# Kernel tuning notes

Measured on AMD Instinct MI355X. Metric: run time of the kernel, lower is better.

Reference implementation:

```python
import jax, jax.numpy as jnp
import numpy as np

B, LQ, LK, E, H = 8, 1024, 1024, 512, 8
D = E // H
NEG = -2.0**32 + 1  # padding value used by original torch code


def setup_inputs() -> dict:
    key = jax.random.key(0)
    ks = jax.random.split(key, 6)
    s = 0.02
    return {
        "x1": jax.random.normal(ks[0], (B, LQ, E), jnp.float32),
        "x2": jax.random.normal(ks[1], (B, LK, E), jnp.float32),
        "Wq": jax.random.normal(ks[2], (E, E), jnp.float32) * s,
        "bq": jnp.zeros((E,), jnp.float32),
        "Wk": jax.random.normal(ks[3], (E, E), jnp.float32) * s,
        "bk": jnp.zeros((E,), jnp.float32),
        "Wv": jax.random.normal(ks[4], (E, E), jnp.float32) * s,
        "bv": jnp.zeros((E,), jnp.float32),
    }


def _split_heads(t):
    # torch: cat(split(t, E//H, dim=2), dim=0) -> head-major [H, B, L, D]
    b, l, _ = t.shape
    return jnp.moveaxis(t.reshape(b, l, H, D), 2, 0)


def reference(x1, x2, Wq, bq, Wk, bk, Wv, bv):
    # ReLU-activated projections (nn.Linear: x @ W.T + b)
    q = jax.nn.relu(x1 @ Wq.T + bq)  # [B,LQ,E]
    k = jax.nn.relu(x2 @ Wk.T + bk)  # [B,LK,E]
    v = jax.nn.relu(x2 @ Wv.T + bv)  # [B,LK,E]

    q_, k_, v_ = _split_heads(q), _split_heads(k), _split_heads(v)  # [H,B,L,D]

    # scaled scores; original scales by sqrt(emb_size), not sqrt(d_head)
    scores = jnp.einsum('hbqd,hbkd->hbqk', q_, k_) / jnp.sqrt(jnp.float32(E))

    # sin-based key mask from raw x2
    key_mask = jnp.sin(jnp.abs(jnp.sum(x2, -1)))  # [B,LK]
    scores = jnp.where(key_mask[None, :, None, :] <= 0, NEG, scores)

    attn = jax.nn.softmax(scores, axis=-1)

    # sin-based query mask from raw x1, applied after softmax
    query_mask = jnp.sin(jnp.abs(jnp.sum(x1, -1)))  # [B,LQ]
    attn = attn * query_mask[None, :, :, None]

    out = jnp.einsum('hbqk,hbkd->hbqd', attn, v_)  # [H,B,LQ,D]
    out = jnp.moveaxis(out, 0, 2).reshape(B, LQ, E)  # merge heads back
    return out + q  # residual add with activated query projection
```

## Files before the change

### kernel.cpp

```cpp
#include <hip/hip_runtime.h>
#include <hip/hip_bf16.h>
#include <math.h>

typedef short bf16x8 __attribute__((ext_vector_type(8)));
typedef float f32x4 __attribute__((ext_vector_type(4)));
typedef unsigned int u32;
typedef unsigned short u16;

constexpr int Bb = 8, LQn = 1024, LKn = 1024, En = 512, Hn = 8, Dn = 64;
constexpr int Mtok = Bb * LQn;
constexpr float KCOEF = 0.06376246332977306f;

__device__ __forceinline__ u16 f2bf(float f) {
  u32 u = __builtin_bit_cast(u32, f);
  u32 r = (u + 0x7fffu + ((u >> 16) & 1u)) >> 16;
  return (u16)r;
}
__device__ __forceinline__ float bf2f(u16 h) {
  u32 u = ((u32)h) << 16;
  return __builtin_bit_cast(float, u);
}
__device__ __forceinline__ u16 f2bf_hw(float f) {
  return __builtin_bit_cast(u16, __float2bfloat16(f));
}

__device__ __forceinline__ void async_lds16(const void* gsrc, void* ldst) {
  __builtin_amdgcn_global_load_lds(
      (const __attribute__((address_space(1))) u32*)gsrc,
      (__attribute__((address_space(3))) u32*)ldst, 16, 0, 0);
}

__global__ void prep_kernel(const float* __restrict__ x1, const float* __restrict__ x2,
                            u16* __restrict__ x1b, u16* __restrict__ x2b,
                            float* __restrict__ qmask, float* __restrict__ kbias,
                            const float* __restrict__ Wq, const float* __restrict__ Wk,
                            const float* __restrict__ Wv, u16* __restrict__ wqb,
                            u16* __restrict__ wkb, u16* __restrict__ wvb) {
  int blk = blockIdx.x;
  if (blk < 4096) {
    int id = blk * 4 + (threadIdx.x >> 6);
    int lane = threadIdx.x & 63;
    const float* x; u16* xb; int row; bool isq;
    if (id < Mtok) { x = x1; xb = x1b; row = id; isq = true; }
    else           { x = x2; xb = x2b; row = id - Mtok; isq = false; }
    const float4* p = reinterpret_cast<const float4*>(x + (size_t)row * En);
    ushort4* ob = reinterpret_cast<ushort4*>(xb + (size_t)row * En);
    double s = 0.0;
#pragma unroll
    for (int j = 0; j < En / 256; ++j) {
      float4 v = p[lane + j * 64];
      s += (double)v.x + (double)v.y + (double)v.z + (double)v.w;
      ushort4 o;
      o.x = f2bf(v.x); o.y = f2bf(v.y); o.z = f2bf(v.z); o.w = f2bf(v.w);
      ob[lane + j * 64] = o;
    }
#pragma unroll
    for (int off = 32; off > 0; off >>= 1) s += __shfl_down(s, off, 64);
    if (lane == 0) {
      float sv = (float)sin(fabs(s));
      if (isq) qmask[row] = sv;
      else     kbias[row] = sv > 0.f ? 0.f : -3.0e38f;
    }
  } else {
    int n4 = En * En / 4;
    int j = (blk - 4096) * 256 + threadIdx.x;
    const float* src; u16* dst;
    if (j < n4) { src = Wq; dst = wqb; }
    else if (j < 2 * n4) { src = Wk; dst = wkb; j -= n4; }
    else { src = Wv; dst = wvb; j -= 2 * n4; }
    float4 v = reinterpret_cast<const float4*>(src)[j];
    ushort4 o;
    o.x = f2bf(v.x); o.y = f2bf(v.y); o.z = f2bf(v.z); o.w = f2bf(v.w);
    reinterpret_cast<ushort4*>(dst)[j] = o;
  }
}

template <int BIAS_ROW>
__device__ __forceinline__ void gemm_core(
    const u16* __restrict__ A, const u16* __restrict__ Bm,
    const float* __restrict__ bias, u16* __restrict__ C,
    int ldc, float coef, int row0, int col0) {
  constexpr int K = 512, BK = 64;
  __shared__ u16 sA[128 * BK];
  __shared__ u16 sB[128 * BK];
  int tid = threadIdx.x;
  int lane = tid & 63;
  int w = tid >> 6;
  int wm = w >> 2, wn = w & 3;
  int rgrp = lane >> 4, cidx = lane & 15;

  f32x4 acc[4][2];
#pragma unroll
  for (int mi = 0; mi < 4; ++mi)
#pragma unroll
    for (int ni = 0; ni < 2; ++ni) acc[mi][ni] = f32x4{0.f, 0.f, 0.f, 0.f};

  for (int kt = 0; kt < K / BK; ++kt) {
    int k0 = kt * BK;
    __syncthreads();
#pragma unroll
    for (int rr = 0; rr < 2; ++rr) {
      int cid = rr * 512 + tid;
      int r = cid >> 3, c = cid & 7;
      int cg = c ^ (r & 7);
      async_lds16(A + (size_t)(row0 + r) * K + k0 + cg * 8, &sA[cid * 8]);
    }
#pragma unroll
    for (int rr = 0; rr < 2; ++rr) {
      int cid = rr * 512 + tid;
      int r = cid >> 3, c = cid & 7;
      int cg = c ^ (r & 7);
      async_lds16(Bm + (size_t)(col0 + r) * K + k0 + cg * 8, &sB[cid * 8]);
    }
    __syncthreads();
#pragma unroll
    for (int kk = 0; kk < 2; ++kk) {
      bf16x8 a[4], b[2];
#pragma unroll
      for (int mi = 0; mi < 4; ++mi) {
        int row = wm * 64 + mi * 16 + cidx;
        a[mi] = *reinterpret_cast<const bf16x8*>(
            &sA[row * BK + ((kk * 4 + rgrp) ^ (row & 7)) * 8]);
      }
#pragma unroll
      for (int ni = 0; ni < 2; ++ni) {
        int row = wn * 32 + ni * 16 + cidx;
        b[ni] = *reinterpret_cast<const bf16x8*>(
            &sB[row * BK + ((kk * 4 + rgrp) ^ (row & 7)) * 8]);
      }
#pragma unroll
      for (int mi = 0; mi < 4; ++mi)
#pragma unroll
        for (int ni = 0; ni < 2; ++ni)
          acc[mi][ni] = __builtin_amdgcn_mfma_f32_16x16x32_bf16(a[mi], b[ni], acc[mi][ni], 0, 0, 0);
    }
  }
#pragma unroll
  for (int mi = 0; mi < 4; ++mi)
#pragma unroll
    for (int ni = 0; ni < 2; ++ni)
#pragma unroll
      for (int r = 0; r < 4; ++r) {
        int grow = row0 + wm * 64 + mi * 16 + rgrp * 4 + r;
        int gcol = col0 + wn * 32 + ni * 16 + cidx;
        float v = acc[mi][ni][r] + (BIAS_ROW ? bias[grow] : bias[gcol]);
        v = v > 0.f ? v : 0.f;
        C[(size_t)grow * ldc + gcol] = f2bf_hw(v * coef);
      }
}

__global__ __launch_bounds__(512, 6) void gemm3(
    const u16* __restrict__ x1b, const u16* __restrict__ wqb, const float* __restrict__ bq,
    u16* __restrict__ qbq,
    const u16* __restrict__ x2b, const u16* __restrict__ wkb, const float* __restrict__ bk,
    u16* __restrict__ kbk,
    const u16* __restrict__ wvb, const float* __restrict__ bv, u16* __restrict__ vtb) {
  int z = blockIdx.z;
  if (z == 0) {
    gemm_core<0>(x1b, wqb, bq, qbq, En, 1.0f, blockIdx.x * 128, blockIdx.y * 128);
  } else if (z == 1) {
    gemm_core<0>(x2b, wkb, bk, kbk, En, KCOEF, blockIdx.x * 128, blockIdx.y * 128);
  } else {
    gemm_core<1>(wvb, x2b, bv, vtb, Mtok, 1.0f, blockIdx.y * 128, blockIdx.x * 128);
  }
}

__global__ __launch_bounds__(256, 4) void attn_kernel(
    const u16* __restrict__ qb, const u16* __restrict__ kb, const u16* __restrict__ vtb,
    const float* __restrict__ kbias, const float* __restrict__ qmask,
    float* __restrict__ out) {
  __shared__ u16 sK[2][64 * 64];
  __shared__ u16 sV[2][64 * 64];
  __shared__ u16 sQP[64 * 64];
  int tid = threadIdx.x, lane = tid & 63, w = tid >> 6;
  int bh = blockIdx.x, qblk = blockIdx.y;
  int b = bh >> 3, h = bh & 7;
  int rgrp = lane >> 4, cidx = lane & 15;

  const u16* qbase = qb + ((size_t)(b * LQn) + qblk * 64) * En + h * Dn;
  const u16* kbase = kb + (size_t)(b * LKn) * En + h * Dn;
  const u16* vbase = vtb + (size_t)(h * Dn) * Mtok + b * LKn;
  const float* kmb = kbias + b * LKn;

  auto stageKV = [&](int kt, int buf) {
#pragma unroll
    for (int rr = 0; rr < 2; ++rr) {
      int cid = rr * 256 + tid;
      int r = cid >> 3, c = cid & 7;
      int cg = c ^ (r & 7);
      async_lds16(kbase + (size_t)(kt * 64 + r) * En + cg * 8, &sK[buf][cid * 8]);
      async_lds16(vbase + (size_t)r * Mtok + kt * 64 + cg * 8, &sV[buf][cid * 8]);
    }
  };

#pragma unroll
  for (int rr = 0; rr < 2; ++rr) {
    int cid = rr * 256 + tid;
    int r = cid >> 3, c = cid & 7;
    int cg = c ^ (r & 7);
    async_lds16(qbase + (size_t)r * En + cg * 8, &sQP[cid * 8]);
  }
  stageKV(0, 0);
  __syncthreads();

  bf16x8 qa0, qa1;
  {
    int row = w * 16 + cidx;
    qa0 = *reinterpret_cast<const bf16x8*>(&sQP[row * 64 + (rgrp ^ (row & 7)) * 8]);
    qa1 = *reinterpret_cast<const bf16x8*>(&sQP[row * 64 + ((4 + rgrp) ^ (row & 7)) * 8]);
  }

  f32x4 acc_o[4];
#pragma unroll
  for (int dt = 0; dt < 4; ++dt) acc_o[dt] = f32x4{0.f, 0.f, 0.f, 0.f};
  float den = 0.f;

  int prow = w * 16 + cidx;
  char* sPbyte = reinterpret_cast<char*>(sQP);

  for (int kt = 0; kt < LKn / 64; ++kt) {
    int cur = kt & 1;
    if (kt < LKn / 64 - 1) stageKV(kt + 1, cur ^ 1);
#pragma unroll
    for (int ktile = 0; ktile < 4; ++ktile) {
      int krow = ktile * 16 + cidx;
      bf16x8 kf0 = *reinterpret_cast<const bf16x8*>(
          &sK[cur][krow * 64 + (rgrp ^ (krow & 7)) * 8]);
      bf16x8 kf1 = *reinterpret_cast<const bf16x8*>(
          &sK[cur][krow * 64 + ((4 + rgrp) ^ (krow & 7)) * 8]);
      float4 km4 = *reinterpret_cast<const float4*>(&kmb[kt * 64 + ktile * 16 + rgrp * 4]);
      f32x4 s;
      s[0] = km4.x; s[1] = km4.y; s[2] = km4.z; s[3] = km4.w;
      s = __builtin_amdgcn_mfma_f32_16x16x32_bf16(kf0, qa0, s, 0, 0, 0);
      s = __builtin_amdgcn_mfma_f32_16x16x32_bf16(kf1, qa1, s, 0, 0, 0);
      float p0 = __builtin_amdgcn_exp2f(s[0]);
      float p1 = __builtin_amdgcn_exp2f(s[1]);
      float p2 = __builtin_amdgcn_exp2f(s[2]);
      float p3 = __builtin_amdgcn_exp2f(s[3]);
      den += (p0 + p1) + (p2 + p3);
      ushort4 pk;
      pk.x = f2bf_hw(p0); pk.y = f2bf_hw(p1); pk.z = f2bf_hw(p2); pk.w = f2bf_hw(p3);
      int gran = ktile * 2 + (rgrp >> 1);
      int boff = prow * 128 + ((gran ^ (prow & 7)) << 4) + ((rgrp & 1) << 3);
      *reinterpret_cast<ushort4*>(sPbyte + boff) = pk;
    }
    __builtin_amdgcn_s_setprio(1);
#pragma unroll
    for (int kk = 0; kk < 2; ++kk) {
      bf16x8 pa = *reinterpret_cast<const bf16x8*>(
          &sQP[prow * 64 + ((kk * 4 + rgrp) ^ (prow & 7)) * 8]);
#pragma unroll
      for (int dt = 0; dt < 4; ++dt) {
        int vrow = dt * 16 + cidx;
        bf16x8 vf = *reinterpret_cast<const bf16x8*>(
            &sV[cur][vrow * 64 + ((kk * 4 + rgrp) ^ (vrow & 7)) * 8]);
        acc_o[dt] = __builtin_amdgcn_mfma_f32_16x16x32_bf16(pa, vf, acc_o[dt], 0, 0, 0);
      }
    }
    __builtin_amdgcn_s_setprio(0);
    __syncthreads();
  }
  den += __shfl_xor(den, 16, 64);
  den += __shfl_xor(den, 32, 64);

  const float* qmb = qmask + (size_t)b * LQn + qblk * 64 + w * 16;
  const u16* qres = qbase + (size_t)(w * 16) * En;
  float* obase = out + ((size_t)(b * LQn) + qblk * 64 + w * 16) * En + h * Dn;
#pragma unroll
  for (int r = 0; r < 4; ++r) {
    int qr = rgrp * 4 + r;
    float denq = __shfl(den, qr, 64);
    float fac = qmb[qr] / denq;
#pragma unroll
    for (int dt = 0; dt < 4; ++dt) {
      float v = acc_o[dt][r] * fac + bf2f(qres[(size_t)qr * En + dt * 16 + cidx]);
      obase[(size_t)qr * En + dt * 16 + cidx] = v;
    }
  }
}

extern "C" void kernel_launch(void* const* d_in, const int* in_sizes, int n_in,
                              void* d_out, int out_size, void* d_ws, size_t ws_size,
                              hipStream_t stream) {
  const float* x1 = (const float*)d_in[0];
  const float* x2 = (const float*)d_in[1];
  const float* Wq = (const float*)d_in[2];
  const float* bq = (const float*)d_in[3];
  const float* Wk = (const float*)d_in[4];
  const float* bk = (const float*)d_in[5];
  const float* Wv = (const float*)d_in[6];
  const float* bv = (const float*)d_in[7];
  float* out = (float*)d_out;

  char* ws = (char*)d_ws;
  size_t o = 0;
  u16* x1b = (u16*)(ws + o); o += (size_t)Mtok * En * 2;
  u16* x2b = (u16*)(ws + o); o += (size_t)Mtok * En * 2;
  u16* wqb = (u16*)(ws + o); o += (size_t)En * En * 2;
  u16* wkb = (u16*)(ws + o); o += (size_t)En * En * 2;
  u16* wvb = (u16*)(ws + o); o += (size_t)En * En * 2;
  u16* qbq = (u16*)(ws + o); o += (size_t)Mtok * En * 2;
  u16* kbk = (u16*)(ws + o); o += (size_t)Mtok * En * 2;
  u16* vtb = (u16*)(ws + o); o += (size_t)Mtok * En * 2;
  float* kbias = (float*)(ws + o); o += (size_t)Mtok * 4;
  float* qmask = (float*)(ws + o); o += (size_t)Mtok * 4;

  prep_kernel<<<4864, 256, 0, stream>>>(x1, x2, x1b, x2b, qmask, kbias,
                                        Wq, Wk, Wv, wqb, wkb, wvb);

  dim3 g3(Mtok / 128, En / 128, 3);
  gemm3<<<g3, 512, 0, stream>>>(x1b, wqb, bq, qbq, x2b, wkb, bk, kbk, wvb, bv, vtb);

  dim3 ga(Bb * Hn, LQn / 64);
  attn_kernel<<<ga, 256, 0, stream>>>(qbq, kbk, vtb, kbias, qmask, out);
}
```

Before: 64.96 us.

## Process 128 query rows per attention block to reuse K/V tiles

```diff
diff --git a/kernel.cpp b/kernel.cpp
--- a/kernel.cpp
+++ b/kernel.cpp
@@ -165,19 +165,19 @@
   }
 }
 
-__global__ __launch_bounds__(256, 4) void attn_kernel(
+__global__ __launch_bounds__(256, 3) void attn_kernel(
     const u16* __restrict__ qb, const u16* __restrict__ kb, const u16* __restrict__ vtb,
     const float* __restrict__ kbias, const float* __restrict__ qmask,
     float* __restrict__ out) {
   __shared__ u16 sK[2][64 * 64];
   __shared__ u16 sV[2][64 * 64];
-  __shared__ u16 sQP[64 * 64];
+  __shared__ u16 sQP[128 * 64];
   int tid = threadIdx.x, lane = tid & 63, w = tid >> 6;
   int bh = blockIdx.x, qblk = blockIdx.y;
   int b = bh >> 3, h = bh & 7;
   int rgrp = lane >> 4, cidx = lane & 15;
 
-  const u16* qbase = qb + ((size_t)(b * LQn) + qblk * 64) * En + h * Dn;
+  const u16* qbase = qb + ((size_t)(b * LQn) + qblk * 128) * En + h * Dn;
   const u16* kbase = kb + (size_t)(b * LKn) * En + h * Dn;
   const u16* vbase = vtb + (size_t)(h * Dn) * Mtok + b * LKn;
   const float* kmb = kbias + b * LKn;
@@ -194,7 +194,7 @@
   };
 
 #pragma unroll
-  for (int rr = 0; rr < 2; ++rr) {
+  for (int rr = 0; rr < 4; ++rr) {
     int cid = rr * 256 + tid;
     int r = cid >> 3, c = cid & 7;
     int cg = c ^ (r & 7);
@@ -203,19 +203,22 @@
   stageKV(0, 0);
   __syncthreads();
 
-  bf16x8 qa0, qa1;
-  {
-    int row = w * 16 + cidx;
-    qa0 = *reinterpret_cast<const bf16x8*>(&sQP[row * 64 + (rgrp ^ (row & 7)) * 8]);
-    qa1 = *reinterpret_cast<const bf16x8*>(&sQP[row * 64 + ((4 + rgrp) ^ (row & 7)) * 8]);
-  }
-
-  f32x4 acc_o[4];
-#pragma unroll
-  for (int dt = 0; dt < 4; ++dt) acc_o[dt] = f32x4{0.f, 0.f, 0.f, 0.f};
-  float den = 0.f;
-
-  int prow = w * 16 + cidx;
+  bf16x8 qa[2][2];
+#pragma unroll
+  for (int g = 0; g < 2; ++g) {
+    int row = g * 64 + w * 16 + cidx;
+    qa[g][0] = *reinterpret_cast<const bf16x8*>(&sQP[row * 64 + (rgrp ^ (row & 7)) * 8]);
+    qa[g][1] = *reinterpret_cast<const bf16x8*>(&sQP[row * 64 + ((4 + rgrp) ^ (row & 7)) * 8]);
+  }
+
+  f32x4 acc_o[2][4];
+#pragma unroll
+  for (int g = 0; g < 2; ++g)
+#pragma unroll
+    for (int dt = 0; dt < 4; ++dt) acc_o[g][dt] = f32x4{0.f, 0.f, 0.f, 0.f};
+  float den0 = 0.f, den1 = 0.f;
+
+  int prow0 = w * 16 + cidx, prow1 = 64 + w * 16 + cidx;
   char* sPbyte = reinterpret_cast<char*>(sQP);
 
   for (int kt = 0; kt < LKn / 64; ++kt) {
@@ -229,52 +232,76 @@
       bf16x8 kf1 = *reinterpret_cast<const bf16x8*>(
           &sK[cur][krow * 64 + ((4 + rgrp) ^ (krow & 7)) * 8]);
       float4 km4 = *reinterpret_cast<const float4*>(&kmb[kt * 64 + ktile * 16 + rgrp * 4]);
-      f32x4 s;
-      s[0] = km4.x; s[1] = km4.y; s[2] = km4.z; s[3] = km4.w;
-      s = __builtin_amdgcn_mfma_f32_16x16x32_bf16(kf0, qa0, s, 0, 0, 0);
-      s = __builtin_amdgcn_mfma_f32_16x16x32_bf16(kf1, qa1, s, 0, 0, 0);
-      float p0 = __builtin_amdgcn_exp2f(s[0]);
-      float p1 = __builtin_amdgcn_exp2f(s[1]);
-      float p2 = __builtin_amdgcn_exp2f(s[2]);
-      float p3 = __builtin_amdgcn_exp2f(s[3]);
-      den += (p0 + p1) + (p2 + p3);
-      ushort4 pk;
-      pk.x = f2bf_hw(p0); pk.y = f2bf_hw(p1); pk.z = f2bf_hw(p2); pk.w = f2bf_hw(p3);
       int gran = ktile * 2 + (rgrp >> 1);
-      int boff = prow * 128 + ((gran ^ (prow & 7)) << 4) + ((rgrp & 1) << 3);
-      *reinterpret_cast<ushort4*>(sPbyte + boff) = pk;
+      {
+        f32x4 s;
+        s[0] = km4.x; s[1] = km4.y; s[2] = km4.z; s[3] = km4.w;
+        s = __builtin_amdgcn_mfma_f32_16x16x32_bf16(kf0, qa[0][0], s, 0, 0, 0);
+        s = __builtin_amdgcn_mfma_f32_16x16x32_bf16(kf1, qa[0][1], s, 0, 0, 0);
+        float p0 = __builtin_amdgcn_exp2f(s[0]);
+        float p1 = __builtin_amdgcn_exp2f(s[1]);
+        float p2 = __builtin_amdgcn_exp2f(s[2]);
+        float p3 = __builtin_amdgcn_exp2f(s[3]);
+        den0 += (p0 + p1) + (p2 + p3);
+        ushort4 pk;
+        pk.x = f2bf_hw(p0); pk.y = f2bf_hw(p1); pk.z = f2bf_hw(p2); pk.w = f2bf_hw(p3);
+        int boff = prow0 * 128 + ((gran ^ (prow0 & 7)) << 4) + ((rgrp & 1) << 3);
+        *reinterpret_cast<ushort4*>(sPbyte + boff) = pk;
+      }
+      {
+        f32x4 s;
+        s[0] = km4.x; s[1] = km4.y; s[2] = km4.z; s[3] = km4.w;
+        s = __builtin_amdgcn_mfma_f32_16x16x32_bf16(kf0, qa[1][0], s, 0, 0, 0);
+        s = __builtin_amdgcn_mfma_f32_16x16x32_bf16(kf1, qa[1][1], s, 0, 0, 0);
+        float p0 = __builtin_amdgcn_exp2f(s[0]);
+        float p1 = __builtin_amdgcn_exp2f(s[1]);
+        float p2 = __builtin_amdgcn_exp2f(s[2]);
+        float p3 = __builtin_amdgcn_exp2f(s[3]);
+        den1 += (p0 + p1) + (p2 + p3);
+        ushort4 pk;
+        pk.x = f2bf_hw(p0); pk.y = f2bf_hw(p1); pk.z = f2bf_hw(p2); pk.w = f2bf_hw(p3);
+        int boff = prow1 * 128 + ((gran ^ (prow1 & 7)) << 4) + ((rgrp & 1) << 3);
+        *reinterpret_cast<ushort4*>(sPbyte + boff) = pk;
+      }
     }
     __builtin_amdgcn_s_setprio(1);
 #pragma unroll
     for (int kk = 0; kk < 2; ++kk) {
-      bf16x8 pa = *reinterpret_cast<const bf16x8*>(
-          &sQP[prow * 64 + ((kk * 4 + rgrp) ^ (prow & 7)) * 8]);
+      bf16x8 pa0 = *reinterpret_cast<const bf16x8*>(
+          &sQP[prow0 * 64 + ((kk * 4 + rgrp) ^ (prow0 & 7)) * 8]);
+      bf16x8 pa1 = *reinterpret_cast<const bf16x8*>(
+          &sQP[prow1 * 64 + ((kk * 4 + rgrp) ^ (prow1 & 7)) * 8]);
 #pragma unroll
       for (int dt = 0; dt < 4; ++dt) {
         int vrow = dt * 16 + cidx;
         bf16x8 vf = *reinterpret_cast<const bf16x8*>(
             &sV[cur][vrow * 64 + ((kk * 4 + rgrp) ^ (vrow & 7)) * 8]);
-        acc_o[dt] = __builtin_amdgcn_mfma_f32_16x16x32_bf16(pa, vf, acc_o[dt], 0, 0, 0);
+        acc_o[0][dt] = __builtin_amdgcn_mfma_f32_16x16x32_bf16(pa0, vf, acc_o[0][dt], 0, 0, 0);
+        acc_o[1][dt] = __builtin_amdgcn_mfma_f32_16x16x32_bf16(pa1, vf, acc_o[1][dt], 0, 0, 0);
       }
     }
     __builtin_amdgcn_s_setprio(0);
     __syncthreads();
   }
-  den += __shfl_xor(den, 16, 64);
-  den += __shfl_xor(den, 32, 64);
-
-  const float* qmb = qmask + (size_t)b * LQn + qblk * 64 + w * 16;
-  const u16* qres = qbase + (size_t)(w * 16) * En;
-  float* obase = out + ((size_t)(b * LQn) + qblk * 64 + w * 16) * En + h * Dn;
-#pragma unroll
-  for (int r = 0; r < 4; ++r) {
-    int qr = rgrp * 4 + r;
-    float denq = __shfl(den, qr, 64);
-    float fac = qmb[qr] / denq;
-#pragma unroll
-    for (int dt = 0; dt < 4; ++dt) {
-      float v = acc_o[dt][r] * fac + bf2f(qres[(size_t)qr * En + dt * 16 + cidx]);
-      obase[(size_t)qr * En + dt * 16 + cidx] = v;
+  den0 += __shfl_xor(den0, 16, 64); den0 += __shfl_xor(den0, 32, 64);
+  den1 += __shfl_xor(den1, 16, 64); den1 += __shfl_xor(den1, 32, 64);
+
+#pragma unroll
+  for (int g = 0; g < 2; ++g) {
+    float den = g ? den1 : den0;
+    const float* qmb = qmask + (size_t)b * LQn + qblk * 128 + g * 64 + w * 16;
+    const u16* qres = qbase + (size_t)(g * 64 + w * 16) * En;
+    float* obase = out + ((size_t)(b * LQn) + qblk * 128 + g * 64 + w * 16) * En + h * Dn;
+#pragma unroll
+    for (int r = 0; r < 4; ++r) {
+      int qr = rgrp * 4 + r;
+      float denq = __shfl(den, qr, 64);
+      float fac = qmb[qr] / denq;
+#pragma unroll
+      for (int dt = 0; dt < 4; ++dt) {
+        float v = acc_o[g][dt][r] * fac + bf2f(qres[(size_t)qr * En + dt * 16 + cidx]);
+        obase[(size_t)qr * En + dt * 16 + cidx] = v;
+      }
     }
   }
 }
@@ -311,6 +338,6 @@
   dim3 g3(Mtok / 128, En / 128, 3);
   gemm3<<<g3, 512, 0, stream>>>(x1b, wqb, bq, qbq, x2b, wkb, bk, kbk, wvb, bv, vtb);
 
-  dim3 ga(Bb * Hn, LQn / 64);
+  dim3 ga(Bb * Hn, LQn / 128);
   attn_kernel<<<ga, 256, 0, stream>>>(qbq, kbk, vtb, kbias, qmask, out);
 }
```

After: 65.85 us. About the same (+1.4%).
